# Kernel tuning notes

Hardware: AMD Instinct MI355X
Metric: run time of the kernel (lower is better)

The kernel has to match this reference:

```python
import jax, jax.numpy as jnp
import numpy as np

EPS = 1e-7  # keras.backend.epsilon()
P = 2       # pool size (both dims)
NUM_STEPS = 3


def _avg_pool(x, p=P):
    # non-overlapping avg pool, H,W divisible by p (== 'same' padding here)
    b, h, w, c = x.shape
    return x.reshape(b, h // p, p, w // p, p, c).mean(axis=(2, 4))


def _max_pool(x, p=P):
    b, h, w, c = x.shape
    return x.reshape(b, h // p, p, w // p, p, c).max(axis=(2, 4))


def _upsample(x, p=P):
    # K.resize_images nearest-neighbor upsampling by factor p
    return jnp.repeat(jnp.repeat(x, p, axis=1), p, axis=2)


def _squash(fm):
    v_len = jnp.linalg.norm(fm, axis=-1, keepdims=True) + EPS
    return fm / (1.0 + v_len)


def _normalize_pool_map(score_map, temperature=2.0):
    max_map = jax.lax.stop_gradient(_upsample(_max_pool(score_map)))
    s = jnp.exp((score_map - max_map) / temperature)
    avg = _upsample(_avg_pool(s))
    return s / (avg + EPS)


def setup_inputs() -> dict:
    key = jax.random.key(0)
    x = jax.random.normal(key, (32, 64, 64, 256), dtype=jnp.float32)
    return {"x": x}


def reference(x) -> jnp.ndarray:
    score_map = None
    weighted_fm = x
    for _ in range(NUM_STEPS):
        if score_map is None:
            weighted_fm = x
        else:
            weighted_fm = _normalize_pool_map(score_map) * x
        avg_fm = _squash(_avg_pool(weighted_fm))
        cols = _upsample(avg_fm)  # back to input resolution
        new_score = jnp.sum(x * cols, axis=-1, keepdims=True)
        score_map = new_score if score_map is None else score_map + new_score
    return _avg_pool(weighted_fm)
```

## Files before the change

kernel.cpp:

```cpp
#include <hip/hip_runtime.h>


static constexpr float EPS = 1e-7f;

__global__ __launch_bounds__(256) void capsule_pool_kernel(
    const float* __restrict__ x, float* __restrict__ out)
{
    constexpr int H = 64, W = 64, C = 256;
    constexpr int HB = H / 2, WB = W / 2;

    const int lane  = threadIdx.x & 63;
    const int waveId = threadIdx.x >> 6;
    const int blk = blockIdx.x * 4 + waveId;

    const int j = blk & (WB - 1);
    const int i = (blk >> 5) & (HB - 1);
    const int b = blk >> 10;

    const size_t rowStride = (size_t)W * C;
    const size_t base = ((size_t)b * H + 2 * i) * rowStride
                      + (size_t)(2 * j) * C + lane * 4;

    const float4 xv0 = *(const float4*)(x + base);
    const float4 xv1 = *(const float4*)(x + base + C);
    const float4 xv2 = *(const float4*)(x + base + rowStride);
    const float4 xv3 = *(const float4*)(x + base + rowStride + C);

    float s0 = 0.f, s1 = 0.f, s2 = 0.f, s3 = 0.f;
    float4 a;

    #pragma unroll
    for (int step = 0; step < 3; ++step) {
        float n0 = 1.f, n1 = 1.f, n2 = 1.f, n3 = 1.f;
        if (step > 0) {
            const float m = fmaxf(fmaxf(s0, s1), fmaxf(s2, s3));
            const float e0 = expf((s0 - m) * 0.5f);
            const float e1 = expf((s1 - m) * 0.5f);
            const float e2 = expf((s2 - m) * 0.5f);
            const float e3 = expf((s3 - m) * 0.5f);
            const float inv = 1.f / (0.25f * (e0 + e1 + e2 + e3) + EPS);
            n0 = e0 * inv; n1 = e1 * inv; n2 = e2 * inv; n3 = e3 * inv;
        }
        a.x = 0.25f * (n0 * xv0.x + n1 * xv1.x + n2 * xv2.x + n3 * xv3.x);
        a.y = 0.25f * (n0 * xv0.y + n1 * xv1.y + n2 * xv2.y + n3 * xv3.y);
        a.z = 0.25f * (n0 * xv0.z + n1 * xv1.z + n2 * xv2.z + n3 * xv3.z);
        a.w = 0.25f * (n0 * xv0.w + n1 * xv1.w + n2 * xv2.w + n3 * xv3.w);

        if (step < 2) {
            float ss = a.x * a.x + a.y * a.y + a.z * a.z + a.w * a.w;
            #pragma unroll
            for (int off = 32; off; off >>= 1) ss += __shfl_xor(ss, off, 64);
            const float scale = 1.f / (1.f + sqrtf(ss) + EPS);

            float p0 = xv0.x * a.x + xv0.y * a.y + xv0.z * a.z + xv0.w * a.w;
            float p1 = xv1.x * a.x + xv1.y * a.y + xv1.z * a.z + xv1.w * a.w;
            float p2 = xv2.x * a.x + xv2.y * a.y + xv2.z * a.z + xv2.w * a.w;
            float p3 = xv3.x * a.x + xv3.y * a.y + xv3.z * a.z + xv3.w * a.w;
            #pragma unroll
            for (int off = 32; off; off >>= 1) {
                p0 += __shfl_xor(p0, off, 64);
                p1 += __shfl_xor(p1, off, 64);
                p2 += __shfl_xor(p2, off, 64);
                p3 += __shfl_xor(p3, off, 64);
            }
            s0 += p0 * scale; s1 += p1 * scale;
            s2 += p2 * scale; s3 += p3 * scale;
        }
    }

    const size_t obase = (((size_t)b * HB + i) * WB + j) * C + lane * 4;
    *(float4*)(out + obase) = a;
}

extern "C" void kernel_launch(void* const* d_in, const int* in_sizes, int n_in,
                              void* d_out, int out_size, void* d_ws, size_t ws_size,
                              hipStream_t stream) {
    const float* x = (const float*)d_in[0];
    float* out = (float*)d_out;
    capsule_pool_kernel<<<8192, 256, 0, stream>>>(x, out);
}
```

Before: 31.74 us.

## Precompute 4x4 Gram matrix once and iterate routing scores algebraically

Computes the 10 unique pairwise dot products of the four pixel vectors with a single set of wave reductions. All routing steps are then evaluated as small scalar algebra on that Gram matrix, which removes the per-step norm and score shuffle reductions. It also adds an occupancy hint to launch bounds and writes the output with a nontemporal store. The change trades 15 per-step shuffle reductions for 10 upfront ones, and the kernel is likely memory-bound, so gains may be limited.

```diff
diff --git a/kernel.cpp b/kernel.cpp
--- a/kernel.cpp
+++ b/kernel.cpp
@@ -3,13 +3,19 @@
 
 static constexpr float EPS = 1e-7f;
 
-__global__ __launch_bounds__(256) void capsule_pool_kernel(
+typedef float f32x4 __attribute__((ext_vector_type(4)));
+
+__device__ __forceinline__ float dot4(const float4& u, const float4& v) {
+    return u.x * v.x + u.y * v.y + u.z * v.z + u.w * v.w;
+}
+
+__global__ __launch_bounds__(256, 8) void capsule_pool_kernel(
     const float* __restrict__ x, float* __restrict__ out)
 {
     constexpr int H = 64, W = 64, C = 256;
     constexpr int HB = H / 2, WB = W / 2;
 
-    const int lane  = threadIdx.x & 63;
+    const int lane   = threadIdx.x & 63;
     const int waveId = threadIdx.x >> 6;
     const int blk = blockIdx.x * 4 + waveId;
 
@@ -18,20 +24,36 @@
     const int b = blk >> 10;
 
     const size_t rowStride = (size_t)W * C;
-    const size_t base = ((size_t)b * H + 2 * i) * rowStride
-                      + (size_t)(2 * j) * C + lane * 4;
+    const float* p = x + ((size_t)b * H + 2 * i) * rowStride
+                       + (size_t)(2 * j) * C + 4 * lane;
 
-    const float4 xv0 = *(const float4*)(x + base);
-    const float4 xv1 = *(const float4*)(x + base + C);
-    const float4 xv2 = *(const float4*)(x + base + rowStride);
-    const float4 xv3 = *(const float4*)(x + base + rowStride + C);
+    const float4 x0 = *(const float4*)(p);
+    const float4 x1 = *(const float4*)(p + C);
+    const float4 x2 = *(const float4*)(p + rowStride);
+    const float4 x3 = *(const float4*)(p + rowStride + C);
+
+    float g00 = dot4(x0, x0), g01 = dot4(x0, x1), g02 = dot4(x0, x2), g03 = dot4(x0, x3);
+    float g11 = dot4(x1, x1), g12 = dot4(x1, x2), g13 = dot4(x1, x3);
+    float g22 = dot4(x2, x2), g23 = dot4(x2, x3), g33 = dot4(x3, x3);
+
+    #pragma unroll
+    for (int off = 1; off < 64; off <<= 1) {
+        g00 += __shfl_xor(g00, off, 64);
+        g01 += __shfl_xor(g01, off, 64);
+        g02 += __shfl_xor(g02, off, 64);
+        g03 += __shfl_xor(g03, off, 64);
+        g11 += __shfl_xor(g11, off, 64);
+        g12 += __shfl_xor(g12, off, 64);
+        g13 += __shfl_xor(g13, off, 64);
+        g22 += __shfl_xor(g22, off, 64);
+        g23 += __shfl_xor(g23, off, 64);
+        g33 += __shfl_xor(g33, off, 64);
+    }
 
     float s0 = 0.f, s1 = 0.f, s2 = 0.f, s3 = 0.f;
-    float4 a;
-
+    float n0 = 1.f, n1 = 1.f, n2 = 1.f, n3 = 1.f;
     #pragma unroll
     for (int step = 0; step < 3; ++step) {
-        float n0 = 1.f, n1 = 1.f, n2 = 1.f, n3 = 1.f;
         if (step > 0) {
             const float m = fmaxf(fmaxf(s0, s1), fmaxf(s2, s3));
             const float e0 = expf((s0 - m) * 0.5f);
@@ -41,35 +63,28 @@
             const float inv = 1.f / (0.25f * (e0 + e1 + e2 + e3) + EPS);
             n0 = e0 * inv; n1 = e1 * inv; n2 = e2 * inv; n3 = e3 * inv;
         }
-        a.x = 0.25f * (n0 * xv0.x + n1 * xv1.x + n2 * xv2.x + n3 * xv3.x);
-        a.y = 0.25f * (n0 * xv0.y + n1 * xv1.y + n2 * xv2.y + n3 * xv3.y);
-        a.z = 0.25f * (n0 * xv0.z + n1 * xv1.z + n2 * xv2.z + n3 * xv3.z);
-        a.w = 0.25f * (n0 * xv0.w + n1 * xv1.w + n2 * xv2.w + n3 * xv3.w);
-
         if (step < 2) {
-            float ss = a.x * a.x + a.y * a.y + a.z * a.z + a.w * a.w;
-            #pragma unroll
-            for (int off = 32; off; off >>= 1) ss += __shfl_xor(ss, off, 64);
-            const float scale = 1.f / (1.f + sqrtf(ss) + EPS);
-
-            float p0 = xv0.x * a.x + xv0.y * a.y + xv0.z * a.z + xv0.w * a.w;
-            float p1 = xv1.x * a.x + xv1.y * a.y + xv1.z * a.z + xv1.w * a.w;
-            float p2 = xv2.x * a.x + xv2.y * a.y + xv2.z * a.z + xv2.w * a.w;
-            float p3 = xv3.x * a.x + xv3.y * a.y + xv3.z * a.z + xv3.w * a.w;
-            #pragma unroll
-            for (int off = 32; off; off >>= 1) {
-                p0 += __shfl_xor(p0, off, 64);
-                p1 += __shfl_xor(p1, off, 64);
-                p2 += __shfl_xor(p2, off, 64);
-                p3 += __shfl_xor(p3, off, 64);
-            }
-            s0 += p0 * scale; s1 += p1 * scale;
-            s2 += p2 * scale; s3 += p3 * scale;
+            const float q0 = n0 * g00 + n1 * g01 + n2 * g02 + n3 * g03;
+            const float q1 = n0 * g01 + n1 * g11 + n2 * g12 + n3 * g13;
+            const float q2 = n0 * g02 + n1 * g12 + n2 * g22 + n3 * g23;
+            const float q3 = n0 * g03 + n1 * g13 + n2 * g23 + n3 * g33;
+            const float aa2 = 0.0625f * (n0 * q0 + n1 * q1 + n2 * q2 + n3 * q3);
+            const float scale = 1.f / (1.f + sqrtf(aa2) + EPS);
+            s0 += 0.25f * q0 * scale;
+            s1 += 0.25f * q1 * scale;
+            s2 += 0.25f * q2 * scale;
+            s3 += 0.25f * q3 * scale;
         }
     }
 
-    const size_t obase = (((size_t)b * HB + i) * WB + j) * C + lane * 4;
-    *(float4*)(out + obase) = a;
+    f32x4 a;
+    a.x = 0.25f * (n0 * x0.x + n1 * x1.x + n2 * x2.x + n3 * x3.x);
+    a.y = 0.25f * (n0 * x0.y + n1 * x1.y + n2 * x2.y + n3 * x3.y);
+    a.z = 0.25f * (n0 * x0.z + n1 * x1.z + n2 * x2.z + n3 * x3.z);
+    a.w = 0.25f * (n0 * x0.w + n1 * x1.w + n2 * x2.w + n3 * x3.w);
+
+    float* o = out + (((size_t)b * HB + i) * WB + j) * C + 4 * lane;
+    __builtin_nontemporal_store(a, (f32x4*)o);
 }
 
 extern "C" void kernel_launch(void* const* d_in, const int* in_sizes, int n_in,
```

After: 32.56 us. +2.6%, slower.
